# Optimization experiments

Measured on AMD Instinct MI355X. Metric: run time of the kernel, lower is better.

Reference implementation:

```python
import jax, jax.numpy as jnp
import numpy as np

B, T, D = 4, 2048, 1024
H = 16
HD = D // H  # 64
SCALE = 1.0 / np.sqrt(HD).astype(np.float32)


def setup_inputs() -> dict:
    key = jax.random.key(0)
    ks = jax.random.split(key, 5)
    std = 0.02
    return {
        "x": jax.random.normal(ks[0], (B, T, D), dtype=jnp.float32),
        "wq": jax.random.normal(ks[1], (D, D), dtype=jnp.float32) * std,
        "wk": jax.random.normal(ks[2], (D, D), dtype=jnp.float32) * std,
        "wv": jax.random.normal(ks[3], (D, D), dtype=jnp.float32) * std,
        "wo": jax.random.normal(ks[4], (D, D), dtype=jnp.float32) * std,
    }


def _shape(t):
    # [B,T,D] -> [B,H,T,HD]
    Bt, Tt, _ = t.shape
    return t.reshape(Bt, Tt, H, HD).transpose(0, 2, 1, 3)


def reference(x, wq, wk, wv, wo):
    # Linear layers are y = x @ W^T (torch nn.Linear semantics, no bias)
    q = _shape(x @ wq.T)  # [B,H,T,HD]
    k = _shape(x @ wk.T)
    v = _shape(x @ wv.T)
    att = jnp.einsum("bhqd,bhkd->bhqk", q, k) * SCALE  # [B,H,T,T]
    # causal mask: -inf strictly above diagonal
    causal = jnp.triu(jnp.full((T, T), -jnp.inf, dtype=att.dtype), k=1)
    att = att + causal[None, None, :, :]
    att = jax.nn.softmax(att.astype(jnp.float32), axis=-1).astype(att.dtype)
    # dropout prob = 0.0 -> identity
    y = jnp.einsum("bhqk,bhkd->bhqd", att, v)  # [B,H,T,HD]
    y = y.transpose(0, 2, 1, 3).reshape(B, T, D)
    return y @ wo.T
```

## Files before the change

kernel.cpp:

```cpp
#include <hip/hip_runtime.h>
#include <hip/hip_bf16.h>

#define BB 4
#define TT 2048
#define DDIM 1024
#define HH 16
#define HD 64

typedef __bf16 bf16_t;
typedef __bf16 bf16x4 __attribute__((ext_vector_type(4)));
typedef __bf16 bf16x8 __attribute__((ext_vector_type(8)));
typedef float f32x4 __attribute__((ext_vector_type(4)));

#define GLOAD_LDS(gp, lp) \
    __builtin_amdgcn_global_load_lds( \
        (const __attribute__((address_space(1))) void*)(gp), \
        (__attribute__((address_space(3))) void*)(lp), 16, 0, 0)

__global__ __launch_bounds__(256) void cvt_f32_bf16(
    const float* __restrict__ src, bf16_t* __restrict__ dst, size_t n8)
{
    size_t i = (size_t)blockIdx.x * blockDim.x + threadIdx.x;
    const size_t stride = (size_t)gridDim.x * blockDim.x;
    for (; i < n8; i += stride) {
        const f32x4 a = ((const f32x4*)src)[2 * i];
        const f32x4 b = ((const f32x4*)src)[2 * i + 1];
        bf16x8 v;
#pragma unroll
        for (int j = 0; j < 4; j++) { v[j] = (bf16_t)a[j]; v[4 + j] = (bf16_t)b[j]; }
        ((bf16x8*)dst)[i] = v;
    }
}

__global__ __launch_bounds__(256) void cvt_wpack(
    const float* __restrict__ s0, const float* __restrict__ s1,
    const float* __restrict__ s2, const float* __restrict__ s3,
    bf16_t* __restrict__ dst)
{
    const size_t n8 = (size_t)4 * DDIM * DDIM / 8;
    size_t i = (size_t)blockIdx.x * blockDim.x + threadIdx.x;
    const size_t stride = (size_t)gridDim.x * blockDim.x;
    for (; i < n8; i += stride) {
        const int sel = (int)(i >> 17);
        const float* s = sel == 0 ? s0 : sel == 1 ? s1 : sel == 2 ? s2 : s3;
        const size_t off8 = i & ((1u << 17) - 1);
        const f32x4 a = ((const f32x4*)s)[2 * off8];
        const f32x4 b = ((const f32x4*)s)[2 * off8 + 1];
        bf16x8 v;
#pragma unroll
        for (int j = 0; j < 4; j++) { v[j] = (bf16_t)a[j]; v[4 + j] = (bf16_t)b[j]; }
        ((bf16x8*)dst)[i] = v;
    }
}

__device__ __forceinline__ void stage8(const bf16_t* __restrict__ g, int ld,
                                       bf16_t* __restrict__ ldsbase, int lane)
{
    const int rr = lane >> 3;
    const int cc = (lane & 7) ^ ((rr & 1) << 2);
    GLOAD_LDS(&g[(size_t)rr * ld + cc * 8], ldsbase);
}

__global__ __launch_bounds__(256) void gemm_qkv(
    const bf16_t* __restrict__ A, const bf16_t* __restrict__ Wqkv,
    bf16_t* __restrict__ Qo, bf16_t* __restrict__ Ko, bf16_t* __restrict__ Vto,
    int M, int K)
{
    __shared__ alignas(16) bf16_t As[128 * 64];
    __shared__ alignas(16) bf16_t Bs[128 * 64];

    const int tid  = threadIdx.x;
    const int lane = tid & 63;
    const int w    = tid >> 6;
    const int quad = lane >> 4;
    const int l15  = lane & 15;
    const int wm   = (w >> 1) * 64;
    const int wn   = (w & 1) * 64;
    const int tileN = blockIdx.x * 128;
    const int tileM = blockIdx.y * 128;

    const f32x4 vzero = {0.f, 0.f, 0.f, 0.f};
    f32x4 acc[4][4];
#pragma unroll
    for (int i = 0; i < 4; i++)
#pragma unroll
        for (int j = 0; j < 4; j++) acc[i][j] = vzero;

    const int par4 = (l15 & 1) << 2;

    for (int k0 = 0; k0 < K; k0 += 64) {
        __syncthreads();
#pragma unroll
        for (int q = 0; q < 4; q++) {
            const int r0 = w * 32 + q * 8;
            stage8(&A[(size_t)(tileM + r0) * K + k0], K, &As[r0 * 64], lane);
            stage8(&Wqkv[(size_t)(tileN + r0) * K + k0], K, &Bs[r0 * 64], lane);
        }
        __syncthreads();

#pragma unroll
        for (int ss = 0; ss < 2; ss++) {
            const int phys = ((ss * 4 + quad) ^ par4) << 3;
            bf16x8 af[4], bf[4];
#pragma unroll
            for (int i = 0; i < 4; i++)
                af[i] = *(bf16x8*)&As[(wm + i * 16 + l15) * 64 + phys];
#pragma unroll
            for (int j = 0; j < 4; j++)
                bf[j] = *(bf16x8*)&Bs[(wn + j * 16 + l15) * 64 + phys];
#pragma unroll
            for (int i = 0; i < 4; i++)
#pragma unroll
                for (int j = 0; j < 4; j++)
                    acc[i][j] = __builtin_amdgcn_mfma_f32_16x16x32_bf16(
                        af[i], bf[j], acc[i][j], 0, 0, 0);
        }
    }

    const int region = tileN >> 10;
#pragma unroll
    for (int i = 0; i < 4; i++) {
        const int row = tileM + wm + i * 16 + quad * 4;
#pragma unroll
        for (int j = 0; j < 4; j++) {
            const int ncol = tileN + wn + j * 16 + l15;
            if (region == 2) {
                const int cl = ncol - 2048;
                const int h = cl >> 6, d = cl & 63;
                const int bb = row >> 11, tloc = row & (TT - 1);
                bf16x4 pk;
#pragma unroll
                for (int r = 0; r < 4; r++) pk[r] = (bf16_t)acc[i][j][r];
                *(bf16x4*)&Vto[(((size_t)bb * HH + h) * HD + d) * TT + tloc] = pk;
            } else {
                bf16_t* dst = (region == 0) ? Qo : Ko;
                const int cl = ncol & 1023;
#pragma unroll
                for (int r = 0; r < 4; r++)
                    dst[(size_t)(row + r) * DDIM + cl] = (bf16_t)acc[i][j][r];
            }
        }
    }
}

__global__ __launch_bounds__(256) void gemm_out(
    const bf16_t* __restrict__ A, const bf16_t* __restrict__ Bm,
    float* __restrict__ C, int M, int N, int K)
{
    __shared__ alignas(16) bf16_t As[64 * 64];
    __shared__ alignas(16) bf16_t Bs[128 * 64];

    const int tid  = threadIdx.x;
    const int lane = tid & 63;
    const int w    = tid >> 6;
    const int quad = lane >> 4;
    const int l15  = lane & 15;
    const int wm   = (w >> 1) * 32;
    const int wn   = (w & 1) * 64;
    const int tileN = blockIdx.x * 128;
    const int tileM = blockIdx.y * 64;

    const f32x4 vzero = {0.f, 0.f, 0.f, 0.f};
    f32x4 acc[2][4];
#pragma unroll
    for (int i = 0; i < 2; i++)
#pragma unroll
        for (int j = 0; j < 4; j++) acc[i][j] = vzero;

    const int par4 = (l15 & 1) << 2;

    for (int k0 = 0; k0 < K; k0 += 64) {
        __syncthreads();
#pragma unroll
        for (int q = 0; q < 2; q++) {
            const int r0 = w * 16 + q * 8;
            stage8(&A[(size_t)(tileM + r0) * K + k0], K, &As[r0 * 64], lane);
        }
#pragma unroll
        for (int q = 0; q < 4; q++) {
            const int r0 = w * 32 + q * 8;
            stage8(&Bm[(size_t)(tileN + r0) * K + k0], K, &Bs[r0 * 64], lane);
        }
        __syncthreads();

#pragma unroll
        for (int ss = 0; ss < 2; ss++) {
            const int phys = ((ss * 4 + quad) ^ par4) << 3;
            bf16x8 af[2], bf[4];
#pragma unroll
            for (int i = 0; i < 2; i++)
                af[i] = *(bf16x8*)&As[(wm + i * 16 + l15) * 64 + phys];
#pragma unroll
            for (int j = 0; j < 4; j++)
                bf[j] = *(bf16x8*)&Bs[(wn + j * 16 + l15) * 64 + phys];
#pragma unroll
            for (int i = 0; i < 2; i++)
#pragma unroll
                for (int j = 0; j < 4; j++)
                    acc[i][j] = __builtin_amdgcn_mfma_f32_16x16x32_bf16(
                        af[i], bf[j], acc[i][j], 0, 0, 0);
        }
    }

#pragma unroll
    for (int i = 0; i < 2; i++) {
#pragma unroll
        for (int r = 0; r < 4; r++) {
            const int row = tileM + wm + i * 16 + quad * 4 + r;
#pragma unroll
            for (int j = 0; j < 4; j++)
                C[(size_t)row * N + tileN + wn + j * 16 + l15] = acc[i][j][r];
        }
    }
}

__global__ __launch_bounds__(256, 2) void attn_causal(
    const bf16_t* __restrict__ Q, const bf16_t* __restrict__ Kg,
    const bf16_t* __restrict__ Vt_g, bf16_t* __restrict__ Y)
{
    __shared__ alignas(16) bf16_t Ks[64 * 72];
    __shared__ alignas(16) bf16_t Vt[64 * 72];
    __shared__ alignas(16) bf16_t Ps[4][32 * 72];

    const int tid  = threadIdx.x;
    const int lane = tid & 63;
    const int w    = tid >> 6;
    const int quad = lane >> 4;
    const int l15  = lane & 15;
    const int bh   = blockIdx.x;
    const int sp   = blockIdx.y;
    const int b = bh >> 4, h = bh & 15;

    const int stg_row = tid >> 3;
    const int stg_c8  = (tid & 7) * 8;

    const f32x4 vzero = {0.f, 0.f, 0.f, 0.f};
    bf16x8 ones;
#pragma unroll
    for (int j = 0; j < 8; j++) ones[j] = (l15 == 0) ? (bf16_t)1.0f : (bf16_t)0.0f;

#pragma unroll 1
    for (int half = 0; half < 2; half++) {
        const int strip = half ? (15 - sp) : sp;
        const int qbase = strip * 128;

        bf16x8 qf[2][2];
#pragma unroll
        for (int mi = 0; mi < 2; mi++) {
            const size_t rq =
                (size_t)(b * TT + qbase + w * 32 + mi * 16 + l15) * DDIM + h * 64;
            qf[mi][0] = *(const bf16x8*)&Q[rq + quad * 8];
            qf[mi][1] = *(const bf16x8*)&Q[rq + 32 + quad * 8];
        }

        f32x4 o[2][4], o4[2];
#pragma unroll
        for (int mi = 0; mi < 2; mi++) {
#pragma unroll
            for (int c = 0; c < 4; c++) o[mi][c] = vzero;
            o4[mi] = vzero;
        }

        const int nkt = 2 * strip + 2;
        for (int kt = 0; kt < nkt; kt++) {
            const int kbase = kt * 64;
            __syncthreads();
#pragma unroll
            for (int p = 0; p < 2; p++) {
                const int r = stg_row + p * 32;
                *(bf16x8*)&Ks[r * 72 + stg_c8] =
                    *(const bf16x8*)&Kg[(size_t)(b * TT + kbase + r) * DDIM + h * 64 + stg_c8];
                *(bf16x8*)&Vt[r * 72 + stg_c8] =
                    *(const bf16x8*)&Vt_g[((size_t)bh * HD + r) * TT + kbase + stg_c8];
            }
            __syncthreads();

            f32x4 s[2][4];
#pragma unroll
            for (int c = 0; c < 4; c++) {
                bf16x8 kf0 = *(bf16x8*)&Ks[(c * 16 + l15) * 72 + quad * 8];
                bf16x8 kf1 = *(bf16x8*)&Ks[(c * 16 + l15) * 72 + 32 + quad * 8];
#pragma unroll
                for (int mi = 0; mi < 2; mi++) {
                    f32x4 t = __builtin_amdgcn_mfma_f32_16x16x32_bf16(
                        qf[mi][0], kf0, vzero, 0, 0, 0);
                    s[mi][c] = __builtin_amdgcn_mfma_f32_16x16x32_bf16(
                        qf[mi][1], kf1, t, 0, 0, 0);
                }
            }

#pragma unroll
            for (int mi = 0; mi < 2; mi++) {
                const int qlow = qbase + w * 32 + mi * 16;
                const bool need = (kbase + 63 > qlow);
#pragma unroll
                for (int r = 0; r < 4; r++) {
                    const int qrow = qlow + quad * 4 + r;
                    const int prow = mi * 16 + quad * 4 + r;
#pragma unroll
                    for (int c = 0; c < 4; c++) {
                        float sv = s[mi][c][r] * 0.125f;
                        if (need && (kbase + c * 16 + l15 > qrow)) sv = -1e30f;
                        const int pchunk = (c * 2 + (l15 >> 3)) ^ (prow >> 2);
                        Ps[w][prow * 72 + (pchunk << 3) + (l15 & 7)] =
                            (bf16_t)__expf(sv);
                    }
                }
            }

#pragma unroll
            for (int ss = 0; ss < 2; ss++) {
                bf16x8 pf[2];
#pragma unroll
                for (int mi = 0; mi < 2; mi++) {
                    const int m = mi * 16 + l15;
                    pf[mi] = *(bf16x8*)&Ps[w][m * 72 +
                                              ((((ss * 4 + quad) ^ (m >> 2)) & 7) << 3)];
                }
#pragma unroll
                for (int c = 0; c < 4; c++) {
                    bf16x8 vf = *(bf16x8*)&Vt[(c * 16 + l15) * 72 + ss * 32 + quad * 8];
#pragma unroll
                    for (int mi = 0; mi < 2; mi++)
                        o[mi][c] = __builtin_amdgcn_mfma_f32_16x16x32_bf16(
                            pf[mi], vf, o[mi][c], 0, 0, 0);
                }
#pragma unroll
                for (int mi = 0; mi < 2; mi++)
                    o4[mi] = __builtin_amdgcn_mfma_f32_16x16x32_bf16(
                        pf[mi], ones, o4[mi], 0, 0, 0);
            }
        }

#pragma unroll
        for (int mi = 0; mi < 2; mi++) {
#pragma unroll
            for (int r = 0; r < 4; r++) {
                const float lsum = __shfl(o4[mi][r], lane & 48, 64);
                const float inv = 1.0f / lsum;
                const int q = qbase + w * 32 + mi * 16 + quad * 4 + r;
#pragma unroll
                for (int c = 0; c < 4; c++)
                    Y[(size_t)(b * TT + q) * DDIM + h * 64 + c * 16 + l15] =
                        (bf16_t)(o[mi][c][r] * inv);
            }
        }
    }
}

extern "C" void kernel_launch(void* const* d_in, const int* in_sizes, int n_in,
                              void* d_out, int out_size, void* d_ws, size_t ws_size,
                              hipStream_t stream) {
    (void)in_sizes; (void)n_in; (void)out_size;
    const float* x  = (const float*)d_in[0];
    float* out = (float*)d_out;

    const int M = BB * TT;
    const size_t REGION = (size_t)M * DDIM;
    const size_t WREG   = (size_t)DDIM * DDIM;
    const size_t BATCH  = (size_t)TT * DDIM;
    bf16_t* ws = (bf16_t*)d_ws;

    if (ws_size >= (72ull << 20)) {
        bf16_t* xb  = ws;
        bf16_t* wpk = ws + REGION;
        bf16_t* Qb  = wpk + 4 * WREG;
        bf16_t* Kb  = Qb + REGION;
        bf16_t* Vtb = Kb + REGION;

        cvt_f32_bf16<<<1024, 256, 0, stream>>>(x, xb, REGION / 8);
        cvt_wpack<<<512, 256, 0, stream>>>(
            (const float*)d_in[1], (const float*)d_in[2],
            (const float*)d_in[3], (const float*)d_in[4], wpk);

        gemm_qkv<<<dim3(24, M / 128), 256, 0, stream>>>(
            xb, wpk, Qb, Kb, Vtb, M, DDIM);
        attn_causal<<<dim3(BB * HH, 8), 256, 0, stream>>>(Qb, Kb, Vtb, Qb);
        gemm_out<<<dim3(8, M / 64), 256, 0, stream>>>(
            Qb, wpk + 3 * WREG, out, M, DDIM, DDIM);
    } else {
        bf16_t* wpk = ws;
        bf16_t* xbb = ws + 4 * WREG;
        bf16_t* Qb  = xbb + BATCH;
        bf16_t* Kb  = Qb + BATCH;
        bf16_t* Vtb = Kb + BATCH;

        cvt_wpack<<<512, 256, 0, stream>>>(
            (const float*)d_in[1], (const float*)d_in[2],
            (const float*)d_in[3], (const float*)d_in[4], wpk);

        for (int b = 0; b < BB; b++) {
            const float* x_b = x + (size_t)b * BATCH;
            float* out_b = out + (size_t)b * BATCH;
            cvt_f32_bf16<<<512, 256, 0, stream>>>(x_b, xbb, BATCH / 8);
            gemm_qkv<<<dim3(24, TT / 128), 256, 0, stream>>>(
                xbb, wpk, Qb, Kb, Vtb, TT, DDIM);
            attn_causal<<<dim3(HH, 8), 256, 0, stream>>>(Qb, Kb, Vtb, Qb);
            gemm_out<<<dim3(8, TT / 64), 256, 0, stream>>>(
                Qb, wpk + 3 * WREG, out_b, TT, DDIM, DDIM);
        }
    }
}
```

Measured before the change: 265.7 us.

## Register-prefetch next K/V tile, use exp2 softmax, raise priority around MFMAs

The attention loop now loads the next K and V^T tile from global memory into registers while the current tile is computed, then writes them to LDS at the start of the next iteration. This is meant to hide global load latency. The exponent is computed with the hardware exp2 and the log2(e) factor folded into the scale, replacing __expf. s_setprio is raised around the MFMA sections so waves in matrix phases get scheduling priority. The prefetch uses more registers, which could lower occupancy.

```diff
diff --git a/kernel.cpp b/kernel.cpp
--- a/kernel.cpp
+++ b/kernel.cpp
@@ -239,6 +239,13 @@
 #pragma unroll
     for (int j = 0; j < 8; j++) ones[j] = (l15 == 0) ? (bf16_t)1.0f : (bf16_t)0.0f;
 
+    const bf16_t* kg0 = &Kg[(size_t)(b * TT + stg_row) * DDIM + h * 64 + stg_c8];
+    const bf16_t* vg0 = &Vt_g[((size_t)bh * HD + stg_row) * TT + stg_c8];
+    bf16_t* ksd = &Ks[stg_row * 72 + stg_c8];
+    bf16_t* vtd = &Vt[stg_row * 72 + stg_c8];
+
+    const float SC_LOG2E = 0.125f * 1.44269504f;
+
 #pragma unroll 1
     for (int half = 0; half < 2; half++) {
         const int strip = half ? (15 - sp) : sp;
@@ -262,20 +269,35 @@
         }
 
         const int nkt = 2 * strip + 2;
+
+        bf16x8 kreg[2], vreg[2];
+#pragma unroll
+        for (int p = 0; p < 2; p++) {
+            kreg[p] = *(const bf16x8*)&kg0[(size_t)(p * 32) * DDIM];
+            vreg[p] = *(const bf16x8*)&vg0[(size_t)(p * 32) * TT];
+        }
+
+#pragma unroll 1
         for (int kt = 0; kt < nkt; kt++) {
             const int kbase = kt * 64;
             __syncthreads();
 #pragma unroll
             for (int p = 0; p < 2; p++) {
-                const int r = stg_row + p * 32;
-                *(bf16x8*)&Ks[r * 72 + stg_c8] =
-                    *(const bf16x8*)&Kg[(size_t)(b * TT + kbase + r) * DDIM + h * 64 + stg_c8];
-                *(bf16x8*)&Vt[r * 72 + stg_c8] =
-                    *(const bf16x8*)&Vt_g[((size_t)bh * HD + r) * TT + kbase + stg_c8];
+                *(bf16x8*)&ksd[p * 32 * 72] = kreg[p];
+                *(bf16x8*)&vtd[p * 32 * 72] = vreg[p];
+            }
+            if (kt + 1 < nkt) {
+                const int nb = (kt + 1) * 64;
+#pragma unroll
+                for (int p = 0; p < 2; p++) {
+                    kreg[p] = *(const bf16x8*)&kg0[(size_t)(nb + p * 32) * DDIM];
+                    vreg[p] = *(const bf16x8*)&vg0[(size_t)(p * 32) * TT + nb];
+                }
             }
             __syncthreads();
 
             f32x4 s[2][4];
+            __builtin_amdgcn_s_setprio(1);
 #pragma unroll
             for (int c = 0; c < 4; c++) {
                 bf16x8 kf0 = *(bf16x8*)&Ks[(c * 16 + l15) * 72 + quad * 8];
@@ -288,6 +310,7 @@
                         qf[mi][1], kf1, t, 0, 0, 0);
                 }
             }
+            __builtin_amdgcn_s_setprio(0);
 
 #pragma unroll
             for (int mi = 0; mi < 2; mi++) {
@@ -299,15 +322,16 @@
                     const int prow = mi * 16 + quad * 4 + r;
 #pragma unroll
                     for (int c = 0; c < 4; c++) {
-                        float sv = s[mi][c][r] * 0.125f;
+                        float sv = s[mi][c][r] * SC_LOG2E;
                         if (need && (kbase + c * 16 + l15 > qrow)) sv = -1e30f;
                         const int pchunk = (c * 2 + (l15 >> 3)) ^ (prow >> 2);
                         Ps[w][prow * 72 + (pchunk << 3) + (l15 & 7)] =
-                            (bf16_t)__expf(sv);
+                            (bf16_t)__builtin_amdgcn_exp2f(sv);
                     }
                 }
             }
 
+            __builtin_amdgcn_s_setprio(1);
 #pragma unroll
             for (int ss = 0; ss < 2; ss++) {
                 bf16x8 pf[2];
@@ -330,6 +354,7 @@
                     o4[mi] = __builtin_amdgcn_mfma_f32_16x16x32_bf16(
                         pf[mi], ones, o4[mi], 0, 0, 0);
             }
+            __builtin_amdgcn_s_setprio(0);
         }
 
 #pragma unroll
```

Result: faster. 258.4 us (-2.7%).
